# Performance work log

Hardware: AMD Instinct MI355X
Metric: run time of the kernel (lower is better)

Reference implementation:

```python
import jax, jax.numpy as jnp
import numpy as np

B, S, DIM = 32, 1, 4096
NH, NKV, HD = 32, 8, 128
N_REP = NH // NKV
MAX_SEQ = 2048
START_POS = 2047


def setup_inputs() -> dict:
    key = jax.random.key(0)
    ks = jax.random.split(key, 10)
    t = jnp.arange(S) + START_POS  # absolute positions of the new tokens
    inv_freq = 1.0 / (10000.0 ** (jnp.arange(0, HD, 2, dtype=jnp.float32) / HD))  # [HD/2]
    angles = t[:, None].astype(jnp.float32) * inv_freq[None, :]  # [S, HD/2]
    return {
        "x": jax.random.normal(ks[0], (B, S, DIM), dtype=jnp.float32),
        "freqs_cos": jnp.cos(angles),
        "freqs_sin": jnp.sin(angles),
        "cache_k": jax.random.normal(ks[1], (B, MAX_SEQ, NKV, HD), dtype=jnp.float32),
        "cache_v": jax.random.normal(ks[2], (B, MAX_SEQ, NKV, HD), dtype=jnp.float32),
        "wq": jax.random.normal(ks[3], (NH * HD, DIM), dtype=jnp.float32) * 0.02,
        "wk": jax.random.normal(ks[4], (NKV * HD, DIM), dtype=jnp.float32) * 0.02,
        "wv": jax.random.normal(ks[5], (NKV * HD, DIM), dtype=jnp.float32) * 0.02,
        "wo": jax.random.normal(ks[6], (NH * HD, DIM), dtype=jnp.float32).T * 0.02,  # stored [out,in]=[DIM, NH*HD]
        "start_pos": START_POS,
    }


def _apply_rope(t, cos, sin):
    # t: [B, S, H, HD]; cos/sin: [S, HD/2] -> broadcast [1, S, 1, HD/2]
    tr = t.reshape(*t.shape[:-1], HD // 2, 2)
    x0, x1 = tr[..., 0], tr[..., 1]
    c = cos[None, :, None, :]
    s = sin[None, :, None, :]
    o0 = x0 * c - x1 * s
    o1 = x0 * s + x1 * c
    return jnp.stack([o0, o1], axis=-1).reshape(t.shape)


def reference(x, freqs_cos, freqs_sin, cache_k, cache_v, wq, wk, wv, wo, start_pos):
    batch, seq_len, _ = x.shape
    xq = jnp.einsum('bsd,ed->bse', x, wq).reshape(batch, seq_len, NH, HD)
    xk = jnp.einsum('bsd,ed->bse', x, wk).reshape(batch, seq_len, NKV, HD)
    xv = jnp.einsum('bsd,ed->bse', x, wv).reshape(batch, seq_len, NKV, HD)

    xq = _apply_rope(xq, freqs_cos, freqs_sin)
    xk = _apply_rope(xk, freqs_cos, freqs_sin)

    # KV-cache scatter-write, then read prefix [0, start_pos+seq_len)
    ck = jax.lax.dynamic_update_slice(cache_k, xk, (0, start_pos, 0, 0))
    cv = jax.lax.dynamic_update_slice(cache_v, xv, (0, start_pos, 0, 0))
    T = start_pos + seq_len  # static Python int
    keys = ck[:, :T]    # [B, T, NKV, HD]
    values = cv[:, :T]  # [B, T, NKV, HD]

    # GQA without materializing repeat_kv: group query heads by kv head
    q = xq.reshape(batch, seq_len, NKV, N_REP, HD)
    scores = jnp.einsum('bsgrd,btgd->bgrst', q, keys) / jnp.sqrt(jnp.float32(HD))
    probs = jax.nn.softmax(scores.astype(jnp.float32), axis=-1).astype(xq.dtype)
    out = jnp.einsum('bgrst,btgd->bsgrd', probs, values)  # [B, S, NKV, N_REP, HD]
    out = out.reshape(batch, seq_len, NH * HD)
    return jnp.einsum('bse,de->bsd', out, wo)
```

## Files before the change

### kernel.cpp

```cpp
#include <hip/hip_runtime.h>
#include <hip/hip_bf16.h>

#define B     32
#define DIM   4096
#define NH    32
#define NKV   8
#define HD    128
#define TCACHE 2048
#define NREP  4
#define SPLIT 8
#define TS    256
#define CHUNK 256

__device__ __forceinline__ void gemm_core_v3(
    const float* __restrict__ inp, const float* __restrict__ W,
    float* __restrict__ outp, int stride, int row0, bool rope,
    const float* __restrict__ fc, const float* __restrict__ fs,
    float (*xs)[B][CHUNK])
{
    const int tid = threadIdx.x;
    const int wid = tid >> 6;
    const int kt  = tid & 63;
    const int rg  = wid >> 1;
    const int bh  = wid & 1;
    const int r0  = row0 + rg * 4;
    const int b0  = bh * 16;

    const float* wp = W + (size_t)r0 * DIM;

    const int sb = tid >> 4;
    const int sc = (tid & 15) * 16;
    const float* sbase = inp + (size_t)sb * DIM + sc;

    float acc[4][16];
#pragma unroll
    for (int r = 0; r < 4; ++r)
#pragma unroll
        for (int b = 0; b < 16; ++b) acc[r][b] = 0.f;

    float4 xr[4], wa[4];
#pragma unroll
    for (int j = 0; j < 4; ++j) xr[j] = *(const float4*)(sbase + j * 4);
#pragma unroll
    for (int r = 0; r < 4; ++r) wa[r] = *(const float4*)(wp + (size_t)r * DIM + kt * 4);
#pragma unroll
    for (int j = 0; j < 4; ++j)
        *(float4*)(&xs[0][sb][sc + j * 4]) = xr[j];

    int buf = 0;
    for (int ch = 0; ch < DIM / CHUNK; ++ch) {
        __syncthreads();
        const bool more = (ch + 1 < DIM / CHUNK);
        float4 wb[4];
        if (more) {
            const int k1 = (ch + 1) * CHUNK;
#pragma unroll
            for (int j = 0; j < 4; ++j) xr[j] = *(const float4*)(sbase + k1 + j * 4);
#pragma unroll
            for (int r = 0; r < 4; ++r) wb[r] = *(const float4*)(wp + k1 + (size_t)r * DIM + kt * 4);
        }
        const float* xrow = &xs[buf][b0][kt * 4];
#pragma unroll
        for (int b = 0; b < 16; ++b) {
            float4 xv = *(const float4*)(xrow + b * CHUNK);
#pragma unroll
            for (int r = 0; r < 4; ++r) {
                acc[r][b] = fmaf(wa[r].x, xv.x, acc[r][b]);
                acc[r][b] = fmaf(wa[r].y, xv.y, acc[r][b]);
                acc[r][b] = fmaf(wa[r].z, xv.z, acc[r][b]);
                acc[r][b] = fmaf(wa[r].w, xv.w, acc[r][b]);
            }
        }
        if (more) {
#pragma unroll
            for (int j = 0; j < 4; ++j)
                *(float4*)(&xs[buf ^ 1][sb][sc + j * 4]) = xr[j];
#pragma unroll
            for (int r = 0; r < 4; ++r) wa[r] = wb[r];
        }
        buf ^= 1;
    }

    float myout = 0.f;
#pragma unroll
    for (int r = 0; r < 4; ++r) {
#pragma unroll
        for (int bb = 0; bb < 16; ++bb) {
            float v = acc[r][bb];
#pragma unroll
            for (int off = 1; off < 64; off <<= 1) v += __shfl_xor(v, off);
            if (kt == r * 16 + bb) myout = v;
        }
    }

    const int orow = kt >> 4;
    const int ob   = b0 + (kt & 15);
    float res;
    if (rope) {
        const float prt = __shfl_xor(myout, 16);
        const int gr = r0 + orow;
        const int fi = (gr & (HD - 1)) >> 1;
        const float c = fc[fi], s = fs[fi];
        res = (gr & 1) ? fmaf(myout, c, prt * s) : fmaf(myout, c, -prt * s);
    } else {
        res = myout;
    }
    outp[(size_t)ob * stride + r0 + orow] = res;
}

__global__ __launch_bounds__(512, 2) void qkv_gemm(
    const float* __restrict__ x,
    const float* __restrict__ wq, const float* __restrict__ wk, const float* __restrict__ wv,
    float* __restrict__ qo, float* __restrict__ ko, float* __restrict__ vo,
    const float* __restrict__ fc, const float* __restrict__ fs)
{
    __shared__ float xs[2][B][CHUNK];
    int blk = blockIdx.x;
    const float* W; float* outp; int stride, row0; bool rope;
    if (blk < 256)      { W = wq; outp = qo; stride = NH * HD;  row0 = blk * 16;         rope = true;  }
    else if (blk < 320) { W = wk; outp = ko; stride = NKV * HD; row0 = (blk - 256) * 16; rope = true;  }
    else                { W = wv; outp = vo; stride = NKV * HD; row0 = (blk - 320) * 16; rope = false; }
    gemm_core_v3(x, W, outp, stride, row0, rope, fc, fs, xs);
}

__global__ __launch_bounds__(512, 2) void gemm_wo(
    const float* __restrict__ inp, const float* __restrict__ W, float* __restrict__ outp)
{
    __shared__ float xs[2][B][CHUNK];
    gemm_core_v3(inp, W, outp, DIM, blockIdx.x * 16, false, nullptr, nullptr, xs);
}

__global__ __launch_bounds__(256) void attn_split_k(
    const float* __restrict__ qr, const float* __restrict__ kn, const float* __restrict__ vn,
    const float* __restrict__ ck, const float* __restrict__ cv,
    float* __restrict__ part_o, float* __restrict__ part_ml)
{
    __shared__ float q_lds[NREP][HD];
    __shared__ float p_lds[TS][NREP];
    __shared__ float red[4][NREP];
    __shared__ float o_scr[8][NREP][HD];

    const int bid = blockIdx.x;
    const int s = bid & 7, h = (bid >> 3) & 7, b = bid >> 6;
    const int t0 = s * TS;
    const int tid = threadIdx.x;

    for (int i = tid; i < NREP * HD; i += 256)
        q_lds[i >> 7][i & 127] = qr[((size_t)b * NH + h * NREP + (i >> 7)) * HD + (i & 127)];
    __syncthreads();

    const int t = t0 + tid;
    const float* kptr = (t == TCACHE - 1)
        ? (kn + ((size_t)b * NKV + h) * HD)
        : (ck + (((size_t)b * TCACHE + t) * NKV + h) * HD);
    float s0 = 0.f, s1 = 0.f, s2 = 0.f, s3 = 0.f;
#pragma unroll 8
    for (int d = 0; d < HD; d += 4) {
        float4 kv = *(const float4*)(kptr + d);
        float4 q0 = *(const float4*)(&q_lds[0][d]);
        float4 q1 = *(const float4*)(&q_lds[1][d]);
        float4 q2 = *(const float4*)(&q_lds[2][d]);
        float4 q3 = *(const float4*)(&q_lds[3][d]);
        s0 = fmaf(q0.x, kv.x, s0); s0 = fmaf(q0.y, kv.y, s0); s0 = fmaf(q0.z, kv.z, s0); s0 = fmaf(q0.w, kv.w, s0);
        s1 = fmaf(q1.x, kv.x, s1); s1 = fmaf(q1.y, kv.y, s1); s1 = fmaf(q1.z, kv.z, s1); s1 = fmaf(q1.w, kv.w, s1);
        s2 = fmaf(q2.x, kv.x, s2); s2 = fmaf(q2.y, kv.y, s2); s2 = fmaf(q2.z, kv.z, s2); s2 = fmaf(q2.w, kv.w, s2);
        s3 = fmaf(q3.x, kv.x, s3); s3 = fmaf(q3.y, kv.y, s3); s3 = fmaf(q3.z, kv.z, s3); s3 = fmaf(q3.w, kv.w, s3);
    }
    const float scale = 0.088388347648318447f;
    s0 *= scale; s1 *= scale; s2 *= scale; s3 *= scale;

    float m0 = s0, m1 = s1, m2 = s2, m3 = s3;
    for (int off = 1; off < 64; off <<= 1) {
        m0 = fmaxf(m0, __shfl_xor(m0, off));
        m1 = fmaxf(m1, __shfl_xor(m1, off));
        m2 = fmaxf(m2, __shfl_xor(m2, off));
        m3 = fmaxf(m3, __shfl_xor(m3, off));
    }
    const int wv_ = tid >> 6, lane = tid & 63;
    if (lane == 0) { red[wv_][0] = m0; red[wv_][1] = m1; red[wv_][2] = m2; red[wv_][3] = m3; }
    __syncthreads();
    m0 = fmaxf(fmaxf(red[0][0], red[1][0]), fmaxf(red[2][0], red[3][0]));
    m1 = fmaxf(fmaxf(red[0][1], red[1][1]), fmaxf(red[2][1], red[3][1]));
    m2 = fmaxf(fmaxf(red[0][2], red[1][2]), fmaxf(red[2][2], red[3][2]));
    m3 = fmaxf(fmaxf(red[0][3], red[1][3]), fmaxf(red[2][3], red[3][3]));
    float p0 = __expf(s0 - m0), p1 = __expf(s1 - m1), p2 = __expf(s2 - m2), p3 = __expf(s3 - m3);
    *(float4*)(&p_lds[tid][0]) = make_float4(p0, p1, p2, p3);
    float l0 = p0, l1 = p1, l2 = p2, l3 = p3;
    for (int off = 1; off < 64; off <<= 1) {
        l0 += __shfl_xor(l0, off);
        l1 += __shfl_xor(l1, off);
        l2 += __shfl_xor(l2, off);
        l3 += __shfl_xor(l3, off);
    }
    __syncthreads();
    if (lane == 0) { red[wv_][0] = l0; red[wv_][1] = l1; red[wv_][2] = l2; red[wv_][3] = l3; }
    __syncthreads();
    if (tid < NREP) {
        float l = red[0][tid] + red[1][tid] + red[2][tid] + red[3][tid];
        float m = (tid == 0) ? m0 : (tid == 1) ? m1 : (tid == 2) ? m2 : m3;
        part_ml[(size_t)bid * 8 + tid * 2]     = m;
        part_ml[(size_t)bid * 8 + tid * 2 + 1] = l;
    }

    const int g  = tid >> 5;
    const int dl = (tid & 31) << 2;
    float4 a0 = make_float4(0,0,0,0), a1 = a0, a2 = a0, a3 = a0;
    const int tb = t0 + g * 32;
#pragma unroll 4
    for (int j = 0; j < 32; ++j) {
        int tt = tb + j;
        const float* vptr = (tt == TCACHE - 1)
            ? (vn + ((size_t)b * NKV + h) * HD)
            : (cv + (((size_t)b * TCACHE + tt) * NKV + h) * HD);
        float4 vvv = *(const float4*)(vptr + dl);
        float4 pp  = *(const float4*)(&p_lds[g * 32 + j][0]);
        a0.x = fmaf(pp.x, vvv.x, a0.x); a0.y = fmaf(pp.x, vvv.y, a0.y); a0.z = fmaf(pp.x, vvv.z, a0.z); a0.w = fmaf(pp.x, vvv.w, a0.w);
        a1.x = fmaf(pp.y, vvv.x, a1.x); a1.y = fmaf(pp.y, vvv.y, a1.y); a1.z = fmaf(pp.y, vvv.z, a1.z); a1.w = fmaf(pp.y, vvv.w, a1.w);
        a2.x = fmaf(pp.z, vvv.x, a2.x); a2.y = fmaf(pp.z, vvv.y, a2.y); a2.z = fmaf(pp.z, vvv.z, a2.z); a2.w = fmaf(pp.z, vvv.w, a2.w);
        a3.x = fmaf(pp.w, vvv.x, a3.x); a3.y = fmaf(pp.w, vvv.y, a3.y); a3.z = fmaf(pp.w, vvv.z, a3.z); a3.w = fmaf(pp.w, vvv.w, a3.w);
    }
    *(float4*)(&o_scr[g][0][dl]) = a0;
    *(float4*)(&o_scr[g][1][dl]) = a1;
    *(float4*)(&o_scr[g][2][dl]) = a2;
    *(float4*)(&o_scr[g][3][dl]) = a3;
    __syncthreads();
    for (int oi = tid; oi < NREP * HD; oi += 256) {
        int r = oi >> 7, d = oi & 127;
        float sum = 0.f;
#pragma unroll
        for (int gg = 0; gg < 8; ++gg) sum += o_scr[gg][r][d];
        part_o[((size_t)bid * NREP + r) * HD + d] = sum;
    }
}

__global__ __launch_bounds__(128) void attn_combine(
    const float* __restrict__ part_o, const float* __restrict__ part_ml,
    float* __restrict__ attn_out)
{
    const int bh = blockIdx.x;
    const int d  = threadIdx.x;
    const int b = bh >> 3, h = bh & 7;
#pragma unroll
    for (int r = 0; r < NREP; ++r) {
        float ms[SPLIT], ls[SPLIT];
        float M = -1e30f;
#pragma unroll
        for (int s = 0; s < SPLIT; ++s) {
            ms[s] = part_ml[(size_t)(bh * SPLIT + s) * 8 + r * 2];
            ls[s] = part_ml[(size_t)(bh * SPLIT + s) * 8 + r * 2 + 1];
            M = fmaxf(M, ms[s]);
        }
        float L = 0.f, o = 0.f;
#pragma unroll
        for (int s = 0; s < SPLIT; ++s) {
            float w = __expf(ms[s] - M);
            L += ls[s] * w;
            o = fmaf(w, part_o[((size_t)(bh * SPLIT + s) * NREP + r) * HD + d], o);
        }
        attn_out[((size_t)b * NH + (h * NREP + r)) * HD + d] = o / L;
    }
}

extern "C" void kernel_launch(void* const* d_in, const int* in_sizes, int n_in,
                              void* d_out, int out_size, void* d_ws, size_t ws_size,
                              hipStream_t stream)
{
    const float* x  = (const float*)d_in[0];
    const float* fc = (const float*)d_in[1];
    const float* fs = (const float*)d_in[2];
    const float* ck = (const float*)d_in[3];
    const float* cv = (const float*)d_in[4];
    const float* wq = (const float*)d_in[5];
    const float* wk = (const float*)d_in[6];
    const float* wv = (const float*)d_in[7];
    const float* wo = (const float*)d_in[8];

    float* ws   = (float*)d_ws;
    float* q_r  = ws;
    float* k_n  = ws + 131072;
    float* v_n  = ws + 163840;
    float* a_o  = ws + 196608;
    float* p_o  = ws + 327680;
    float* p_ml = ws + 1376256;
    float* outp = (float*)d_out;

    qkv_gemm<<<dim3(384), dim3(512), 0, stream>>>(x, wq, wk, wv, q_r, k_n, v_n, fc, fs);
    attn_split_k<<<dim3(B * NKV * SPLIT), dim3(256), 0, stream>>>(q_r, k_n, v_n, ck, cv, p_o, p_ml);
    attn_combine<<<dim3(B * NKV), dim3(128), 0, stream>>>(p_o, p_ml, a_o);
    gemm_wo<<<dim3(256), dim3(512), 0, stream>>>(a_o, wo, outp);
}
```

Before: 211.2 us.

## Fuse split-K attention and combine into one 1024-thread block per head

Replaces the split-K attention kernel (2048 blocks of 256 threads) plus the separate combine kernel with a single kernel that runs one 1024-thread block per (batch, kv-head) and covers the full 2048-token sequence. Each thread computes two key scores, the softmax max and sum are reduced across 16 waves in LDS, and the normalized output is written directly. This removes one launch and the partial-output round trip through global memory. In exchange the grid shrinks to 256 large blocks with about 40KB of LDS each, which lowers parallelism and latency hiding for the bandwidth-bound KV-cache read.

```diff
diff --git a/kernel.cpp b/kernel.cpp
--- a/kernel.cpp
+++ b/kernel.cpp
@@ -8,8 +8,6 @@
 #define HD    128
 #define TCACHE 2048
 #define NREP  4
-#define SPLIT 8
-#define TS    256
 #define CHUNK 256
 
 __device__ __forceinline__ void gemm_core_v3(
@@ -130,134 +128,131 @@
     gemm_core_v3(inp, W, outp, DIM, blockIdx.x * 16, false, nullptr, nullptr, xs);
 }
 
-__global__ __launch_bounds__(256) void attn_split_k(
+__global__ __launch_bounds__(1024) void attn_fused(
     const float* __restrict__ qr, const float* __restrict__ kn, const float* __restrict__ vn,
     const float* __restrict__ ck, const float* __restrict__ cv,
-    float* __restrict__ part_o, float* __restrict__ part_ml)
+    float* __restrict__ attn_out)
 {
     __shared__ float q_lds[NREP][HD];
-    __shared__ float p_lds[TS][NREP];
-    __shared__ float red[4][NREP];
-    __shared__ float o_scr[8][NREP][HD];
-
-    const int bid = blockIdx.x;
-    const int s = bid & 7, h = (bid >> 3) & 7, b = bid >> 6;
-    const int t0 = s * TS;
+    __shared__ float p_lds[NREP][TCACHE];
+    __shared__ float redm[16][NREP];
+    __shared__ float redl[16][NREP];
+    __shared__ float o_scr[16][NREP][HD];
+
+    const int bh = blockIdx.x;
+    const int b = bh >> 3, h = bh & 7;
     const int tid = threadIdx.x;
-
-    for (int i = tid; i < NREP * HD; i += 256)
+    const int w = tid >> 6, lane = tid & 63;
+
+    for (int i = tid; i < NREP * HD; i += 1024)
         q_lds[i >> 7][i & 127] = qr[((size_t)b * NH + h * NREP + (i >> 7)) * HD + (i & 127)];
     __syncthreads();
 
-    const int t = t0 + tid;
-    const float* kptr = (t == TCACHE - 1)
-        ? (kn + ((size_t)b * NKV + h) * HD)
-        : (ck + (((size_t)b * TCACHE + t) * NKV + h) * HD);
-    float s0 = 0.f, s1 = 0.f, s2 = 0.f, s3 = 0.f;
+    const float* kb   = ck + ((size_t)b * TCACHE * NKV + h) * HD;
+    const float* knew = kn + ((size_t)b * NKV + h) * HD;
+    const float* kp0 = kb + (size_t)tid * (NKV * HD);
+    const float* kp1 = (tid + 1024 == TCACHE - 1) ? knew
+                       : kb + (size_t)(tid + 1024) * (NKV * HD);
+
+    float sA0 = 0.f, sA1 = 0.f, sA2 = 0.f, sA3 = 0.f;
+    float sB0 = 0.f, sB1 = 0.f, sB2 = 0.f, sB3 = 0.f;
 #pragma unroll 8
     for (int d = 0; d < HD; d += 4) {
-        float4 kv = *(const float4*)(kptr + d);
+        float4 k0 = *(const float4*)(kp0 + d);
+        float4 k1 = *(const float4*)(kp1 + d);
         float4 q0 = *(const float4*)(&q_lds[0][d]);
         float4 q1 = *(const float4*)(&q_lds[1][d]);
         float4 q2 = *(const float4*)(&q_lds[2][d]);
         float4 q3 = *(const float4*)(&q_lds[3][d]);
-        s0 = fmaf(q0.x, kv.x, s0); s0 = fmaf(q0.y, kv.y, s0); s0 = fmaf(q0.z, kv.z, s0); s0 = fmaf(q0.w, kv.w, s0);
-        s1 = fmaf(q1.x, kv.x, s1); s1 = fmaf(q1.y, kv.y, s1); s1 = fmaf(q1.z, kv.z, s1); s1 = fmaf(q1.w, kv.w, s1);
-        s2 = fmaf(q2.x, kv.x, s2); s2 = fmaf(q2.y, kv.y, s2); s2 = fmaf(q2.z, kv.z, s2); s2 = fmaf(q2.w, kv.w, s2);
-        s3 = fmaf(q3.x, kv.x, s3); s3 = fmaf(q3.y, kv.y, s3); s3 = fmaf(q3.z, kv.z, s3); s3 = fmaf(q3.w, kv.w, s3);
+        sA0 = fmaf(q0.x, k0.x, sA0); sA0 = fmaf(q0.y, k0.y, sA0); sA0 = fmaf(q0.z, k0.z, sA0); sA0 = fmaf(q0.w, k0.w, sA0);
+        sA1 = fmaf(q1.x, k0.x, sA1); sA1 = fmaf(q1.y, k0.y, sA1); sA1 = fmaf(q1.z, k0.z, sA1); sA1 = fmaf(q1.w, k0.w, sA1);
+        sA2 = fmaf(q2.x, k0.x, sA2); sA2 = fmaf(q2.y, k0.y, sA2); sA2 = fmaf(q2.z, k0.z, sA2); sA2 = fmaf(q2.w, k0.w, sA2);
+        sA3 = fmaf(q3.x, k0.x, sA3); sA3 = fmaf(q3.y, k0.y, sA3); sA3 = fmaf(q3.z, k0.z, sA3); sA3 = fmaf(q3.w, k0.w, sA3);
+        sB0 = fmaf(q0.x, k1.x, sB0); sB0 = fmaf(q0.y, k1.y, sB0); sB0 = fmaf(q0.z, k1.z, sB0); sB0 = fmaf(q0.w, k1.w, sB0);
+        sB1 = fmaf(q1.x, k1.x, sB1); sB1 = fmaf(q1.y, k1.y, sB1); sB1 = fmaf(q1.z, k1.z, sB1); sB1 = fmaf(q1.w, k1.w, sB1);
+        sB2 = fmaf(q2.x, k1.x, sB2); sB2 = fmaf(q2.y, k1.y, sB2); sB2 = fmaf(q2.z, k1.z, sB2); sB2 = fmaf(q2.w, k1.w, sB2);
+        sB3 = fmaf(q3.x, k1.x, sB3); sB3 = fmaf(q3.y, k1.y, sB3); sB3 = fmaf(q3.z, k1.z, sB3); sB3 = fmaf(q3.w, k1.w, sB3);
     }
     const float scale = 0.088388347648318447f;
-    s0 *= scale; s1 *= scale; s2 *= scale; s3 *= scale;
-
-    float m0 = s0, m1 = s1, m2 = s2, m3 = s3;
+    sA0 *= scale; sA1 *= scale; sA2 *= scale; sA3 *= scale;
+    sB0 *= scale; sB1 *= scale; sB2 *= scale; sB3 *= scale;
+
+    float m0 = fmaxf(sA0, sB0), m1 = fmaxf(sA1, sB1);
+    float m2 = fmaxf(sA2, sB2), m3 = fmaxf(sA3, sB3);
     for (int off = 1; off < 64; off <<= 1) {
         m0 = fmaxf(m0, __shfl_xor(m0, off));
         m1 = fmaxf(m1, __shfl_xor(m1, off));
         m2 = fmaxf(m2, __shfl_xor(m2, off));
         m3 = fmaxf(m3, __shfl_xor(m3, off));
     }
-    const int wv_ = tid >> 6, lane = tid & 63;
-    if (lane == 0) { red[wv_][0] = m0; red[wv_][1] = m1; red[wv_][2] = m2; red[wv_][3] = m3; }
-    __syncthreads();
-    m0 = fmaxf(fmaxf(red[0][0], red[1][0]), fmaxf(red[2][0], red[3][0]));
-    m1 = fmaxf(fmaxf(red[0][1], red[1][1]), fmaxf(red[2][1], red[3][1]));
-    m2 = fmaxf(fmaxf(red[0][2], red[1][2]), fmaxf(red[2][2], red[3][2]));
-    m3 = fmaxf(fmaxf(red[0][3], red[1][3]), fmaxf(red[2][3], red[3][3]));
-    float p0 = __expf(s0 - m0), p1 = __expf(s1 - m1), p2 = __expf(s2 - m2), p3 = __expf(s3 - m3);
-    *(float4*)(&p_lds[tid][0]) = make_float4(p0, p1, p2, p3);
-    float l0 = p0, l1 = p1, l2 = p2, l3 = p3;
+    if (lane == 0) { redm[w][0] = m0; redm[w][1] = m1; redm[w][2] = m2; redm[w][3] = m3; }
+    __syncthreads();
+    m0 = redm[0][0]; m1 = redm[0][1]; m2 = redm[0][2]; m3 = redm[0][3];
+#pragma unroll
+    for (int ww = 1; ww < 16; ++ww) {
+        m0 = fmaxf(m0, redm[ww][0]);
+        m1 = fmaxf(m1, redm[ww][1]);
+        m2 = fmaxf(m2, redm[ww][2]);
+        m3 = fmaxf(m3, redm[ww][3]);
+    }
+    float pA0 = __expf(sA0 - m0), pA1 = __expf(sA1 - m1), pA2 = __expf(sA2 - m2), pA3 = __expf(sA3 - m3);
+    float pB0 = __expf(sB0 - m0), pB1 = __expf(sB1 - m1), pB2 = __expf(sB2 - m2), pB3 = __expf(sB3 - m3);
+    p_lds[0][tid] = pA0; p_lds[1][tid] = pA1; p_lds[2][tid] = pA2; p_lds[3][tid] = pA3;
+    p_lds[0][tid + 1024] = pB0; p_lds[1][tid + 1024] = pB1;
+    p_lds[2][tid + 1024] = pB2; p_lds[3][tid + 1024] = pB3;
+    float l0 = pA0 + pB0, l1 = pA1 + pB1, l2 = pA2 + pB2, l3 = pA3 + pB3;
     for (int off = 1; off < 64; off <<= 1) {
         l0 += __shfl_xor(l0, off);
         l1 += __shfl_xor(l1, off);
         l2 += __shfl_xor(l2, off);
         l3 += __shfl_xor(l3, off);
     }
-    __syncthreads();
-    if (lane == 0) { red[wv_][0] = l0; red[wv_][1] = l1; red[wv_][2] = l2; red[wv_][3] = l3; }
-    __syncthreads();
-    if (tid < NREP) {
-        float l = red[0][tid] + red[1][tid] + red[2][tid] + red[3][tid];
-        float m = (tid == 0) ? m0 : (tid == 1) ? m1 : (tid == 2) ? m2 : m3;
-        part_ml[(size_t)bid * 8 + tid * 2]     = m;
-        part_ml[(size_t)bid * 8 + tid * 2 + 1] = l;
+    if (lane == 0) { redl[w][0] = l0; redl[w][1] = l1; redl[w][2] = l2; redl[w][3] = l3; }
+    __syncthreads();
+    l0 = 0.f; l1 = 0.f; l2 = 0.f; l3 = 0.f;
+#pragma unroll
+    for (int ww = 0; ww < 16; ++ww) {
+        l0 += redl[ww][0]; l1 += redl[ww][1]; l2 += redl[ww][2]; l3 += redl[ww][3];
     }
 
     const int g  = tid >> 5;
     const int dl = (tid & 31) << 2;
+    const float* vb   = cv + ((size_t)b * TCACHE * NKV + h) * HD;
+    const float* vnew = vn + ((size_t)b * NKV + h) * HD;
     float4 a0 = make_float4(0,0,0,0), a1 = a0, a2 = a0, a3 = a0;
-    const int tb = t0 + g * 32;
+    const int rb = g * 64;
 #pragma unroll 4
-    for (int j = 0; j < 32; ++j) {
-        int tt = tb + j;
-        const float* vptr = (tt == TCACHE - 1)
-            ? (vn + ((size_t)b * NKV + h) * HD)
-            : (cv + (((size_t)b * TCACHE + tt) * NKV + h) * HD);
-        float4 vvv = *(const float4*)(vptr + dl);
-        float4 pp  = *(const float4*)(&p_lds[g * 32 + j][0]);
-        a0.x = fmaf(pp.x, vvv.x, a0.x); a0.y = fmaf(pp.x, vvv.y, a0.y); a0.z = fmaf(pp.x, vvv.z, a0.z); a0.w = fmaf(pp.x, vvv.w, a0.w);
-        a1.x = fmaf(pp.y, vvv.x, a1.x); a1.y = fmaf(pp.y, vvv.y, a1.y); a1.z = fmaf(pp.y, vvv.z, a1.z); a1.w = fmaf(pp.y, vvv.w, a1.w);
-        a2.x = fmaf(pp.z, vvv.x, a2.x); a2.y = fmaf(pp.z, vvv.y, a2.y); a2.z = fmaf(pp.z, vvv.z, a2.z); a2.w = fmaf(pp.z, vvv.w, a2.w);
-        a3.x = fmaf(pp.w, vvv.x, a3.x); a3.y = fmaf(pp.w, vvv.y, a3.y); a3.z = fmaf(pp.w, vvv.z, a3.z); a3.w = fmaf(pp.w, vvv.w, a3.w);
-    }
-    *(float4*)(&o_scr[g][0][dl]) = a0;
-    *(float4*)(&o_scr[g][1][dl]) = a1;
-    *(float4*)(&o_scr[g][2][dl]) = a2;
-    *(float4*)(&o_scr[g][3][dl]) = a3;
-    __syncthreads();
-    for (int oi = tid; oi < NREP * HD; oi += 256) {
-        int r = oi >> 7, d = oi & 127;
+    for (int j = 0; j < 64; ++j) {
+        const int r = rb + j;
+        const float* vp = (r == TCACHE - 1) ? vnew : vb + (size_t)r * (NKV * HD);
+        float4 vv = *(const float4*)(vp + dl);
+        float p0 = p_lds[0][r], p1 = p_lds[1][r], p2 = p_lds[2][r], p3 = p_lds[3][r];
+        a0.x = fmaf(p0, vv.x, a0.x); a0.y = fmaf(p0, vv.y, a0.y); a0.z = fmaf(p0, vv.z, a0.z); a0.w = fmaf(p0, vv.w, a0.w);
+        a1.x = fmaf(p1, vv.x, a1.x); a1.y = fmaf(p1, vv.y, a1.y); a1.z = fmaf(p1, vv.z, a1.z); a1.w = fmaf(p1, vv.w, a1.w);
+        a2.x = fmaf(p2, vv.x, a2.x); a2.y = fmaf(p2, vv.y, a2.y); a2.z = fmaf(p2, vv.z, a2.z); a2.w = fmaf(p2, vv.w, a2.w);
+        a3.x = fmaf(p3, vv.x, a3.x); a3.y = fmaf(p3, vv.y, a3.y); a3.z = fmaf(p3, vv.z, a3.z); a3.w = fmaf(p3, vv.w, a3.w);
+    }
+#pragma unroll
+    for (int c = 0; c < 1; ++c) {}
+    a0.x += __shfl_xor(a0.x, 32); a0.y += __shfl_xor(a0.y, 32); a0.z += __shfl_xor(a0.z, 32); a0.w += __shfl_xor(a0.w, 32);
+    a1.x += __shfl_xor(a1.x, 32); a1.y += __shfl_xor(a1.y, 32); a1.z += __shfl_xor(a1.z, 32); a1.w += __shfl_xor(a1.w, 32);
+    a2.x += __shfl_xor(a2.x, 32); a2.y += __shfl_xor(a2.y, 32); a2.z += __shfl_xor(a2.z, 32); a2.w += __shfl_xor(a2.w, 32);
+    a3.x += __shfl_xor(a3.x, 32); a3.y += __shfl_xor(a3.y, 32); a3.z += __shfl_xor(a3.z, 32); a3.w += __shfl_xor(a3.w, 32);
+    if (lane < 32) {
+        *(float4*)(&o_scr[w][0][dl]) = a0;
+        *(float4*)(&o_scr[w][1][dl]) = a1;
+        *(float4*)(&o_scr[w][2][dl]) = a2;
+        *(float4*)(&o_scr[w][3][dl]) = a3;
+    }
+    __syncthreads();
+
+    if (tid < NREP * HD) {
+        const int hh = tid >> 7, d = tid & 127;
         float sum = 0.f;
 #pragma unroll
-        for (int gg = 0; gg < 8; ++gg) sum += o_scr[gg][r][d];
-        part_o[((size_t)bid * NREP + r) * HD + d] = sum;
-    }
-}
-
-__global__ __launch_bounds__(128) void attn_combine(
-    const float* __restrict__ part_o, const float* __restrict__ part_ml,
-    float* __restrict__ attn_out)
-{
-    const int bh = blockIdx.x;
-    const int d  = threadIdx.x;
-    const int b = bh >> 3, h = bh & 7;
-#pragma unroll
-    for (int r = 0; r < NREP; ++r) {
-        float ms[SPLIT], ls[SPLIT];
-        float M = -1e30f;
-#pragma unroll
-        for (int s = 0; s < SPLIT; ++s) {
-            ms[s] = part_ml[(size_t)(bh * SPLIT + s) * 8 + r * 2];
-            ls[s] = part_ml[(size_t)(bh * SPLIT + s) * 8 + r * 2 + 1];
-            M = fmaxf(M, ms[s]);
-        }
-        float L = 0.f, o = 0.f;
-#pragma unroll
-        for (int s = 0; s < SPLIT; ++s) {
-            float w = __expf(ms[s] - M);
-            L += ls[s] * w;
-            o = fmaf(w, part_o[((size_t)(bh * SPLIT + s) * NREP + r) * HD + d], o);
-        }
-        attn_out[((size_t)b * NH + (h * NREP + r)) * HD + d] = o / L;
+        for (int ww = 0; ww < 16; ++ww) sum += o_scr[ww][hh][d];
+        const float li = (hh == 0) ? l0 : (hh == 1) ? l1 : (hh == 2) ? l2 : l3;
+        attn_out[((size_t)b * NH + h * NREP + hh) * HD + d] = sum / li;
     }
 }
 
@@ -280,12 +275,9 @@
     float* k_n  = ws + 131072;
     float* v_n  = ws + 163840;
     float* a_o  = ws + 196608;
-    float* p_o  = ws + 327680;
-    float* p_ml = ws + 1376256;
     float* outp = (float*)d_out;
 
     qkv_gemm<<<dim3(384), dim3(512), 0, stream>>>(x, wq, wk, wv, q_r, k_n, v_n, fc, fs);
-    attn_split_k<<<dim3(B * NKV * SPLIT), dim3(256), 0, stream>>>(q_r, k_n, v_n, ck, cv, p_o, p_ml);
-    attn_combine<<<dim3(B * NKV), dim3(128), 0, stream>>>(p_o, p_ml, a_o);
+    attn_fused<<<dim3(B * NKV), dim3(1024), 0, stream>>>(q_r, k_n, v_n, ck, cv, a_o);
     gemm_wo<<<dim3(256), dim3(512), 0, stream>>>(a_o, wo, outp);
 }
```

Measured after the change: 337.5 us. +59.8%, slower.
